# Kernel optimization log

Hardware: AMD Instinct MI355X
Metric: run time of the kernel (lower is better)

The kernel has to match this reference:

```python
import jax, jax.numpy as jnp
import numpy as np

L, D, H, F, V, B, S = 4, 256, 8, 2048, 1024, 4, 1024
HD = D // H
EPS = 1e-5
PARAM_NAMES = ['enc_qkv_w','enc_qkv_b','enc_out_w','enc_out_b','enc_ff1_w','enc_ff1_b','enc_ff2_w','enc_ff2_b','enc_ln1_g','enc_ln1_b','enc_ln2_g','enc_ln2_b','dec_sa_qkv_w','dec_sa_qkv_b','dec_sa_out_w','dec_sa_out_b','dec_ca_qkv_w','dec_ca_qkv_b','dec_ca_out_w','dec_ca_out_b','dec_ff1_w','dec_ff1_b','dec_ff2_w','dec_ff2_b','dec_ln1_g','dec_ln1_b','dec_ln2_g','dec_ln2_b','dec_ln3_g','dec_ln3_b']

def _ln(x, g, b):
    m = jnp.mean(x, -1, keepdims=True)
    v = jnp.mean((x - m) ** 2, -1, keepdims=True)
    return (x - m) * jax.lax.rsqrt(v + EPS) * g + b

def _mha(q_in, kv_in, qkv_w, qkv_b, out_w, out_b, key_mask=None):
    wq, wk, wv = jnp.split(qkv_w, 3, axis=0)
    bq, bk, bv = jnp.split(qkv_b, 3, axis=0)
    q = (q_in @ wq.T + bq).reshape(q_in.shape[0], -1, H, HD)
    k = (kv_in @ wk.T + bk).reshape(kv_in.shape[0], -1, H, HD)
    v = (kv_in @ wv.T + bv).reshape(kv_in.shape[0], -1, H, HD)
    scores = jnp.einsum('bqhd,bkhd->bhqk', q, k) / np.float32(np.sqrt(HD))
    if key_mask is not None:
        scores = jnp.where(key_mask[:, None, None, :], jnp.float32(-1e9), scores)
    attn = jax.nn.softmax(scores, axis=-1)
    o = jnp.einsum('bhqk,bkhd->bqhd', attn, v).reshape(q_in.shape[0], -1, D)
    return o @ out_w.T + out_b

def _forward(x, mask, codebook, pos, p):
    h = codebook[x] + pos[:, :x.shape[1], :]  # [B,S,D]
    # --- bidirectional encoder (post-LN, ReLU FFN, torch defaults) ---
    ctx = h
    for l in range(L):
        sa = _mha(ctx, ctx, p['enc_qkv_w'][l], p['enc_qkv_b'][l], p['enc_out_w'][l], p['enc_out_b'][l], mask)
        ctx = _ln(ctx + sa, p['enc_ln1_g'][l], p['enc_ln1_b'][l])
        ff = jax.nn.relu(ctx @ p['enc_ff1_w'][l].T + p['enc_ff1_b'][l]) @ p['enc_ff2_w'][l].T + p['enc_ff2_b'][l]
        ctx = _ln(ctx + ff, p['enc_ln2_g'][l], p['enc_ln2_b'][l])
    # --- depth decoder: original loops per position with tgt len 1.
    # Self-attn over a single token == out_proj(v_proj(x)); cross-attn over the
    # shared context is independent per position, so all S positions batch exactly. ---
    d = h
    for l in range(L):
        wv = p['dec_sa_qkv_w'][l][2 * D:]
        bv = p['dec_sa_qkv_b'][l][2 * D:]
        sa = (d @ wv.T + bv) @ p['dec_sa_out_w'][l].T + p['dec_sa_out_b'][l]
        d = _ln(d + sa, p['dec_ln1_g'][l], p['dec_ln1_b'][l])
        ca = _mha(d, ctx, p['dec_ca_qkv_w'][l], p['dec_ca_qkv_b'][l], p['dec_ca_out_w'][l], p['dec_ca_out_b'][l])
        d = _ln(d + ca, p['dec_ln2_g'][l], p['dec_ln2_b'][l])
        ff = jax.nn.relu(d @ p['dec_ff1_w'][l].T + p['dec_ff1_b'][l]) @ p['dec_ff2_w'][l].T + p['dec_ff2_b'][l]
        d = _ln(d + ff, p['dec_ln3_g'][l], p['dec_ln3_b'][l])
    return d

def setup_inputs() -> dict:
    key = jax.random.key(0)
    ctr = [0]
    def nk():
        k = jax.random.fold_in(key, ctr[0]); ctr[0] += 1; return k
    def prm(shape):
        return jax.random.normal(nk(), shape, jnp.float32) * 0.02
    inp = {
        'x': jax.random.randint(nk(), (B, S), 0, V),
        'mask': jnp.zeros((B, S), bool),
        'codebook': prm((V, D)),
        'pos': prm((1, V, D)),
        'enc_qkv_w': prm((L, 3 * D, D)), 'enc_qkv_b': jnp.zeros((L, 3 * D)),
        'enc_out_w': prm((L, D, D)), 'enc_out_b': jnp.zeros((L, D)),
        'enc_ff1_w': prm((L, F, D)), 'enc_ff1_b': jnp.zeros((L, F)),
        'enc_ff2_w': prm((L, D, F)), 'enc_ff2_b': jnp.zeros((L, D)),
        'enc_ln1_g': jnp.ones((L, D)), 'enc_ln1_b': jnp.zeros((L, D)),
        'enc_ln2_g': jnp.ones((L, D)), 'enc_ln2_b': jnp.zeros((L, D)),
        'dec_sa_qkv_w': prm((L, 3 * D, D)), 'dec_sa_qkv_b': jnp.zeros((L, 3 * D)),
        'dec_sa_out_w': prm((L, D, D)), 'dec_sa_out_b': jnp.zeros((L, D)),
        'dec_ca_qkv_w': prm((L, 3 * D, D)), 'dec_ca_qkv_b': jnp.zeros((L, 3 * D)),
        'dec_ca_out_w': prm((L, D, D)), 'dec_ca_out_b': jnp.zeros((L, D)),
        'dec_ff1_w': prm((L, F, D)), 'dec_ff1_b': jnp.zeros((L, F)),
        'dec_ff2_w': prm((L, D, F)), 'dec_ff2_b': jnp.zeros((L, D)),
        'dec_ln1_g': jnp.ones((L, D)), 'dec_ln1_b': jnp.zeros((L, D)),
        'dec_ln2_g': jnp.ones((L, D)), 'dec_ln2_b': jnp.zeros((L, D)),
        'dec_ln3_g': jnp.ones((L, D)), 'dec_ln3_b': jnp.zeros((L, D)),
    }
    return inp

def reference(x, mask, codebook, pos, enc_qkv_w, enc_qkv_b, enc_out_w, enc_out_b, enc_ff1_w, enc_ff1_b, enc_ff2_w, enc_ff2_b, enc_ln1_g, enc_ln1_b, enc_ln2_g, enc_ln2_b, dec_sa_qkv_w, dec_sa_qkv_b, dec_sa_out_w, dec_sa_out_b, dec_ca_qkv_w, dec_ca_qkv_b, dec_ca_out_w, dec_ca_out_b, dec_ff1_w, dec_ff1_b, dec_ff2_w, dec_ff2_b, dec_ln1_g, dec_ln1_b, dec_ln2_g, dec_ln2_b, dec_ln3_g, dec_ln3_b):
    vals = (enc_qkv_w, enc_qkv_b, enc_out_w, enc_out_b, enc_ff1_w, enc_ff1_b, enc_ff2_w, enc_ff2_b, enc_ln1_g, enc_ln1_b, enc_ln2_g, enc_ln2_b, dec_sa_qkv_w, dec_sa_qkv_b, dec_sa_out_w, dec_sa_out_b, dec_ca_qkv_w, dec_ca_qkv_b, dec_ca_out_w, dec_ca_out_b, dec_ff1_w, dec_ff1_b, dec_ff2_w, dec_ff2_b, dec_ln1_g, dec_ln1_b, dec_ln2_g, dec_ln2_b, dec_ln3_g, dec_ln3_b)
    p = dict(zip(PARAM_NAMES, vals))
    return _forward(x, mask, codebook, pos, p)
```

## Files before the change

### kernel.cpp

```cpp
#include <hip/hip_runtime.h>

typedef unsigned short u16;
typedef unsigned int   u32;
typedef short short8 __attribute__((ext_vector_type(8)));
typedef float f32x4  __attribute__((ext_vector_type(4)));

#define DEV static __device__ __forceinline__

static constexpr int S_ = 1024;
static constexpr int D_ = 256;
static constexpr int NR = 4096;

DEV u16 f2bf(float x) {
    u32 u = __float_as_uint(x);
    return (u16)((u + 0x7FFFu + ((u >> 16) & 1u)) >> 16);
}
DEV float bf2f(u16 s) { return __uint_as_float(((u32)s) << 16); }


__global__ __launch_bounds__(256) void k_fillf(float* __restrict__ o, int n, float v) {
    int i = blockIdx.x * 256 + threadIdx.x;
    if (i < n) o[i] = v;
}

__global__ __launch_bounds__(256) void k_conv_all(
        const float* __restrict__ s0, const float* __restrict__ s1, const float* __restrict__ s2,
        const float* __restrict__ s3, const float* __restrict__ s4, const float* __restrict__ s5,
        const float* __restrict__ s6, const float* __restrict__ s7, const float* __restrict__ s8,
        const float* __restrict__ s9, u16* __restrict__ dst) {
    constexpr int c0 = 786432/4,            c1 = c0 + 262144/4,  c2 = c1 + 2097152/4,
                  c3 = c2 + 2097152/4,      c4 = c3 + 786432/4,  c5 = c4 + 262144/4,
                  c6 = c5 + 786432/4,       c7 = c6 + 262144/4,  c8 = c7 + 2097152/4,
                  c9 = c8 + 2097152/4;
    for (int i = blockIdx.x * 256 + threadIdx.x; i < c9; i += gridDim.x * 256) {
        const float* src; int base;
        if      (i < c0) { src = s0; base = 0;  }
        else if (i < c1) { src = s1; base = c0; }
        else if (i < c2) { src = s2; base = c1; }
        else if (i < c3) { src = s3; base = c2; }
        else if (i < c4) { src = s4; base = c3; }
        else if (i < c5) { src = s5; base = c4; }
        else if (i < c6) { src = s6; base = c5; }
        else if (i < c7) { src = s7; base = c6; }
        else if (i < c8) { src = s8; base = c7; }
        else             { src = s9; base = c8; }
        float4 v = ((const float4*)src)[i - base];
        ushort4 o; o.x = f2bf(v.x); o.y = f2bf(v.y); o.z = f2bf(v.z); o.w = f2bf(v.w);
        ((ushort4*)dst)[i] = o;
    }
}

__global__ __launch_bounds__(256) void k_wsa(const float* __restrict__ qkvw, const float* __restrict__ qkvb,
                                             const float* __restrict__ outw, const float* __restrict__ outb,
                                             u16* __restrict__ wsa, float* __restrict__ bsa) {
    int l = blockIdx.x >> 8, n = blockIdx.x & 255, t = threadIdx.x;
    const float* wv = qkvw + (size_t)l * 196608 + 131072;
    const float* bv = qkvb + l * 768 + 512;
    const float* wo = outw + (size_t)l * 65536 + n * 256;
    float acc = 0.0f, pb = 0.0f;
    for (int j = 0; j < 256; j++) {
        float woj = wo[j];
        acc = fmaf(woj, wv[j * 256 + t], acc);
        pb  = fmaf(woj, bv[j], pb);
    }
    wsa[(size_t)l * 65536 + n * 256 + t] = f2bf(acc);
    if (t == 0) bsa[l * 256 + n] = pb + outb[l * 256 + n];
}

__global__ __launch_bounds__(256) void k_embed(const int* __restrict__ xx,
                                               const float* __restrict__ cb,
                                               const float* __restrict__ pos,
                                               const unsigned char* __restrict__ mask,
                                               float* __restrict__ hf, u16* __restrict__ hb,
                                               float* __restrict__ av, float* __restrict__ avz) {
    int wid = threadIdx.x >> 6, lane = threadIdx.x & 63;
    int row = blockIdx.x * 4 + wid;
    int sp = row & (S_ - 1);
    int tok = xx[row];
    float4 c = ((const float4*)(cb + (size_t)tok * D_))[lane];
    float4 p = ((const float4*)(pos + (size_t)sp * D_))[lane];
    float4 s; s.x = c.x + p.x; s.y = c.y + p.y; s.z = c.z + p.z; s.w = c.w + p.w;
    ((float4*)(hf + (size_t)row * D_))[lane] = s;
    ushort4 o; o.x = f2bf(s.x); o.y = f2bf(s.y); o.z = f2bf(s.z); o.w = f2bf(s.w);
    ((ushort4*)(hb + (size_t)row * D_))[lane] = o;
    if (lane == 0) { av[row] = mask[row] ? -2.0e9f : 0.0f; avz[row] = 0.0f; }
}

__global__ __launch_bounds__(256) void k_ln4(const float* __restrict__ x, const u16* __restrict__ yp,
                                             const float* __restrict__ gg, const float* __restrict__ bb,
                                             float* __restrict__ of, u16* __restrict__ ob) {
    int wid = threadIdx.x >> 6, lane = threadIdx.x & 63;
    int row = blockIdx.x * 4 + wid;
    float4 xv = ((const float4*)(x + (size_t)row * D_))[lane];
    float4 s = xv;
    #pragma unroll
    for (int kz = 0; kz < 4; kz++) {
        ushort4 yv = ((const ushort4*)(yp + (size_t)kz * NR * D_ + (size_t)row * D_))[lane];
        s.x += bf2f(yv.x); s.y += bf2f(yv.y); s.z += bf2f(yv.z); s.w += bf2f(yv.w);
    }
    float sum = s.x + s.y + s.z + s.w;
    float sq  = s.x * s.x + s.y * s.y + s.z * s.z + s.w * s.w;
    #pragma unroll
    for (int m = 1; m < 64; m <<= 1) { sum += __shfl_xor(sum, m, 64); sq += __shfl_xor(sq, m, 64); }
    float mean = sum * (1.0f / 256.0f);
    float var  = sq * (1.0f / 256.0f) - mean * mean;
    float rs = rsqrtf(var + 1e-5f);
    float4 gv = ((const float4*)gg)[lane];
    float4 bv = ((const float4*)bb)[lane];
    float4 o;
    o.x = (s.x - mean) * rs * gv.x + bv.x;
    o.y = (s.y - mean) * rs * gv.y + bv.y;
    o.z = (s.z - mean) * rs * gv.z + bv.z;
    o.w = (s.w - mean) * rs * gv.w + bv.w;
    ((float4*)(of + (size_t)row * D_))[lane] = o;
    ushort4 ub; ub.x = f2bf(o.x); ub.y = f2bf(o.y); ub.z = f2bf(o.z); ub.w = f2bf(o.w);
    ((ushort4*)(ob + (size_t)row * D_))[lane] = ub;
}


template <int BM, int BN, bool RELU, bool OBF16>
__global__ __launch_bounds__(256) void k_gemm(const u16* __restrict__ A, const u16* __restrict__ Bw,
                                              const float* __restrict__ bias,
                                              float* __restrict__ Cf, u16* __restrict__ Cb,
                                              int Nn, int Kk) {
    constexpr int FM = BM / 32, FN = BN / 32;
    constexpr int LDA = 72;
    __shared__ __align__(16) u16 As[BM * LDA];
    __shared__ __align__(16) u16 Bs[BN * LDA];
    int tid = threadIdx.x, w = tid >> 6, lane = tid & 63;
    int lr = lane & 15, g = lane >> 4;
    int wm = w >> 1, wn = w & 1;
    int nbn = Nn / BN;
    int bid = blockIdx.x, nwg = gridDim.x;
    if ((nwg & 7) == 0) bid = (bid & 7) * (nwg >> 3) + (bid >> 3);
    int m0 = (bid / nbn) * BM, n0 = (bid % nbn) * BN;
    int trow = tid >> 3, tcol = (tid & 7) << 3;

    f32x4 acc[FM][FN] = {};

    for (int kb = 0; kb < Kk; kb += 64) {
        if (kb) __syncthreads();
        #pragma unroll
        for (int r = 0; r < BM / 32; r++) {
            int row = r * 32 + trow;
            uint4 v = *(const uint4*)(A + (size_t)(m0 + row) * Kk + kb + tcol);
            *(uint4*)(As + row * LDA + tcol) = v;
        }
        #pragma unroll
        for (int r = 0; r < BN / 32; r++) {
            int row = r * 32 + trow;
            uint4 v = *(const uint4*)(Bw + (size_t)(n0 + row) * Kk + kb + tcol);
            *(uint4*)(Bs + row * LDA + tcol) = v;
        }
        __syncthreads();
        #pragma unroll
        for (int kk = 0; kk < 2; kk++) {
            short8 af[FM], bfr[FN];
            #pragma unroll
            for (int mi = 0; mi < FM; mi++)
                af[mi] = *(const short8*)(As + (wm * (BM / 2) + mi * 16 + lr) * LDA + kk * 32 + g * 8);
            #pragma unroll
            for (int ni = 0; ni < FN; ni++)
                bfr[ni] = *(const short8*)(Bs + (wn * (BN / 2) + ni * 16 + lr) * LDA + kk * 32 + g * 8);
            #pragma unroll
            for (int mi = 0; mi < FM; mi++)
                #pragma unroll
                for (int ni = 0; ni < FN; ni++)
                    acc[mi][ni] = __builtin_amdgcn_mfma_f32_16x16x32_bf16(af[mi], bfr[ni], acc[mi][ni], 0, 0, 0);
        }
    }

    #pragma unroll
    for (int ni = 0; ni < FN; ni++) {
        int col = n0 + wn * (BN / 2) + ni * 16 + lr;
        float bi = bias[col];
        #pragma unroll
        for (int mi = 0; mi < FM; mi++) {
            #pragma unroll
            for (int jj = 0; jj < 4; jj++) {
                int row = m0 + wm * (BM / 2) + mi * 16 + g * 4 + jj;
                float v = acc[mi][ni][jj] + bi;
                if (RELU) v = fmaxf(v, 0.0f);
                if (OBF16) Cb[(size_t)row * Nn + col] = f2bf(v);
                else       Cf[(size_t)row * Nn + col] = v;
            }
        }
    }
}

__global__ __launch_bounds__(256) void k_gemm_ln(const u16* __restrict__ A, const u16* __restrict__ Bw,
                                                 const float* __restrict__ bias,
                                                 const float* __restrict__ resid,
                                                 const float* __restrict__ gg, const float* __restrict__ bb,
                                                 float* __restrict__ of, u16* __restrict__ ob) {
    constexpr int LDA = 72, Kk = 256;
    __shared__ __align__(16) u16 As[16 * LDA];
    __shared__ __align__(16) u16 Bs[256 * LDA];
    int tid = threadIdx.x, w = tid >> 6, lane = tid & 63;
    int lr = lane & 15, g = lane >> 4;
    int bid = blockIdx.x;
    bid = (bid & 7) * 32 + (bid >> 3);
    int m0 = bid * 16;
    int trow = tid >> 3, tcol = (tid & 7) << 3;

    f32x4 acc[4] = {};

    for (int kb = 0; kb < Kk; kb += 64) {
        if (kb) __syncthreads();
        if (tid < 128) {
            int row = tid >> 3;
            uint4 v = *(const uint4*)(A + (size_t)(m0 + row) * Kk + kb + tcol);
            *(uint4*)(As + row * LDA + tcol) = v;
        }
        #pragma unroll
        for (int r = 0; r < 8; r++) {
            int row = r * 32 + trow;
            uint4 v = *(const uint4*)(Bw + (size_t)row * Kk + kb + tcol);
            *(uint4*)(Bs + row * LDA + tcol) = v;
        }
        __syncthreads();
        #pragma unroll
        for (int kk = 0; kk < 2; kk++) {
            short8 af = *(const short8*)(As + lr * LDA + kk * 32 + g * 8);
            #pragma unroll
            for (int ni = 0; ni < 4; ni++) {
                short8 bfr = *(const short8*)(Bs + (w * 64 + ni * 16 + lr) * LDA + kk * 32 + g * 8);
                acc[ni] = __builtin_amdgcn_mfma_f32_16x16x32_bf16(af, bfr, acc[ni], 0, 0, 0);
            }
        }
    }

    __syncthreads();
    float* Cs = (float*)Bs;
    #pragma unroll
    for (int ni = 0; ni < 4; ni++) {
        int col = w * 64 + ni * 16 + lr;
        float bi = bias[col];
        #pragma unroll
        for (int jj = 0; jj < 4; jj++)
            Cs[(g * 4 + jj) * 260 + col] = acc[ni][jj] + bi;
    }
    __syncthreads();

    int row = tid >> 4, c0 = (tid & 15) * 16;
    float v[16];
    float sum = 0.0f, sq = 0.0f;
    #pragma unroll
    for (int i = 0; i < 4; i++) {
        float4 cv = *(float4*)(Cs + row * 260 + c0 + i * 4);
        float4 rv = *(const float4*)(resid + (size_t)(m0 + row) * D_ + c0 + i * 4);
        v[4*i]   = cv.x + rv.x; v[4*i+1] = cv.y + rv.y;
        v[4*i+2] = cv.z + rv.z; v[4*i+3] = cv.w + rv.w;
    }
    #pragma unroll
    for (int i = 0; i < 16; i++) { sum += v[i]; sq += v[i] * v[i]; }
    #pragma unroll
    for (int m = 1; m < 16; m <<= 1) { sum += __shfl_xor(sum, m, 64); sq += __shfl_xor(sq, m, 64); }
    float mean = sum * (1.0f / 256.0f);
    float var  = sq * (1.0f / 256.0f) - mean * mean;
    float rs = rsqrtf(var + 1e-5f);
    float* op = of + (size_t)(m0 + row) * D_ + c0;
    u16*   bp = ob + (size_t)(m0 + row) * D_ + c0;
    #pragma unroll
    for (int i = 0; i < 4; i++) {
        float4 gv = *(const float4*)(gg + c0 + i * 4);
        float4 bv = *(const float4*)(bb + c0 + i * 4);
        float4 o;
        o.x = (v[4*i]   - mean) * rs * gv.x + bv.x;
        o.y = (v[4*i+1] - mean) * rs * gv.y + bv.y;
        o.z = (v[4*i+2] - mean) * rs * gv.z + bv.z;
        o.w = (v[4*i+3] - mean) * rs * gv.w + bv.w;
        *(float4*)(op + i * 4) = o;
        ushort4 ub; ub.x = f2bf(o.x); ub.y = f2bf(o.y); ub.z = f2bf(o.z); ub.w = f2bf(o.w);
        *(ushort4*)(bp + i * 4) = ub;
    }
}

__global__ __launch_bounds__(256) void k_gemm2(const u16* __restrict__ A0, const u16* __restrict__ W0,
                                               const float* __restrict__ b0, u16* __restrict__ C0,
                                               const u16* __restrict__ A1, const u16* __restrict__ W1,
                                               const float* __restrict__ b1, u16* __restrict__ C1) {
    constexpr int LDA = 72, Kk = 256;
    __shared__ __align__(16) u16 As[64 * LDA];
    __shared__ __align__(16) u16 Bs[64 * LDA];
    int tid = threadIdx.x, w = tid >> 6, lane = tid & 63;
    int lr = lane & 15, g = lane >> 4;
    int wm = w >> 1, wn = w & 1;
    int bid = blockIdx.x;
    bid = (bid & 7) * 96 + (bid >> 3);
    const u16 *A, *Bw; const float* bias; u16* Cb; int Nn, nbn, seg;
    if (bid < 256) { A = A0; Bw = W0; bias = b0; Cb = C0; Nn = 256; nbn = 4; seg = bid; }
    else           { A = A1; Bw = W1; bias = b1; Cb = C1; Nn = 512; nbn = 8; seg = bid - 256; }
    int m0 = (seg / nbn) * 64, n0 = (seg % nbn) * 64;
    int trow = tid >> 3, tcol = (tid & 7) << 3;

    f32x4 acc[2][2] = {};

    for (int kb = 0; kb < Kk; kb += 64) {
        if (kb) __syncthreads();
        #pragma unroll
        for (int r = 0; r < 2; r++) {
            int row = r * 32 + trow;
            uint4 va = *(const uint4*)(A + (size_t)(m0 + row) * Kk + kb + tcol);
            *(uint4*)(As + row * LDA + tcol) = va;
            uint4 vb = *(const uint4*)(Bw + (size_t)(n0 + row) * Kk + kb + tcol);
            *(uint4*)(Bs + row * LDA + tcol) = vb;
        }
        __syncthreads();
        #pragma unroll
        for (int kk = 0; kk < 2; kk++) {
            short8 af[2], bfr[2];
            #pragma unroll
            for (int mi = 0; mi < 2; mi++)
                af[mi] = *(const short8*)(As + (wm * 32 + mi * 16 + lr) * LDA + kk * 32 + g * 8);
            #pragma unroll
            for (int ni = 0; ni < 2; ni++)
                bfr[ni] = *(const short8*)(Bs + (wn * 32 + ni * 16 + lr) * LDA + kk * 32 + g * 8);
            #pragma unroll
            for (int mi = 0; mi < 2; mi++)
                #pragma unroll
                for (int ni = 0; ni < 2; ni++)
                    acc[mi][ni] = __builtin_amdgcn_mfma_f32_16x16x32_bf16(af[mi], bfr[ni], acc[mi][ni], 0, 0, 0);
        }
    }

    #pragma unroll
    for (int ni = 0; ni < 2; ni++) {
        int col = n0 + wn * 32 + ni * 16 + lr;
        float bi = bias[col];
        #pragma unroll
        for (int mi = 0; mi < 2; mi++)
            #pragma unroll
            for (int jj = 0; jj < 4; jj++) {
                int row = m0 + wm * 32 + mi * 16 + g * 4 + jj;
                Cb[(size_t)row * Nn + col] = f2bf(acc[mi][ni][jj] + bi);
            }
    }
}

__global__ __launch_bounds__(256) void k_gemm_sk4(const u16* __restrict__ A, const u16* __restrict__ Bw,
                                                  const float* __restrict__ bias, u16* __restrict__ Cp) {
    constexpr int LDA = 72, Nn = 256, Kk = 2048;
    __shared__ __align__(16) u16 As[64 * LDA];
    __shared__ __align__(16) u16 Bs[64 * LDA];
    int tid = threadIdx.x, w = tid >> 6, lane = tid & 63;
    int lr = lane & 15, g = lane >> 4;
    int wm = w >> 1, wn = w & 1;
    int kz = blockIdx.x >> 8;
    int mn = blockIdx.x & 255;
    mn = (mn & 7) * 32 + (mn >> 3);
    int m0 = (mn >> 2) * 64, n0 = (mn & 3) * 64;
    int kbeg = kz * 512;
    int trow = tid >> 3, tcol = (tid & 7) << 3;

    f32x4 acc[2][2] = {};

    for (int kb = kbeg; kb < kbeg + 512; kb += 64) {
        if (kb != kbeg) __syncthreads();
        #pragma unroll
        for (int r = 0; r < 2; r++) {
            int row = r * 32 + trow;
            uint4 va = *(const uint4*)(A + (size_t)(m0 + row) * Kk + kb + tcol);
            *(uint4*)(As + row * LDA + tcol) = va;
            uint4 vb = *(const uint4*)(Bw + (size_t)(n0 + row) * Kk + kb + tcol);
            *(uint4*)(Bs + row * LDA + tcol) = vb;
        }
        __syncthreads();
        #pragma unroll
        for (int kk = 0; kk < 2; kk++) {
            short8 af[2], bfr[2];
            #pragma unroll
            for (int mi = 0; mi < 2; mi++)
                af[mi] = *(const short8*)(As + (wm * 32 + mi * 16 + lr) * LDA + kk * 32 + g * 8);
            #pragma unroll
            for (int ni = 0; ni < 2; ni++)
                bfr[ni] = *(const short8*)(Bs + (wn * 32 + ni * 16 + lr) * LDA + kk * 32 + g * 8);
            #pragma unroll
            for (int mi = 0; mi < 2; mi++)
                #pragma unroll
                for (int ni = 0; ni < 2; ni++)
                    acc[mi][ni] = __builtin_amdgcn_mfma_f32_16x16x32_bf16(af[mi], bfr[ni], acc[mi][ni], 0, 0, 0);
        }
    }

    u16* Cz = Cp + (size_t)kz * NR * Nn;
    #pragma unroll
    for (int ni = 0; ni < 2; ni++) {
        int col = n0 + wn * 32 + ni * 16 + lr;
        float bi = (kz == 0) ? bias[col] : 0.0f;
        #pragma unroll
        for (int mi = 0; mi < 2; mi++)
            #pragma unroll
            for (int jj = 0; jj < 4; jj++) {
                int row = m0 + wm * 32 + mi * 16 + g * 4 + jj;
                Cz[(size_t)row * Nn + col] = f2bf(acc[mi][ni][jj] + bi);
            }
    }
}


__global__ __launch_bounds__(256) void k_attn(const u16* __restrict__ qp, int qs,
                                              const u16* __restrict__ kvp, int ks, int koff, int voff,
                                              const float* __restrict__ addv, u16* __restrict__ out) {
    __shared__ __align__(16) u16 Kl[2][128 * 32];
    __shared__ __align__(16) u16 VTl[2][32 * 136];
    __shared__ __align__(16) u16 Pl[4 * 16 * 136];
    __shared__ float Al[2][128];

    int tid = threadIdx.x, w = tid >> 6, lane = tid & 63;
    int lr = lane & 15, g = lane >> 4;
    int blk = blockIdx.x;
    blk = (blk & 7) * 64 + (blk >> 3);
    int qb = blk & 15, h = (blk >> 4) & 7, b = blk >> 7;
    int q0 = qb * 64 + w * 16;
    const float QS2 = 0.17677669529663687f * 1.4426950408889634f;

    short8 qf = *(const short8*)(qp + (size_t)(b * S_ + q0 + lr) * qs + h * 32 + g * 8);

    f32x4 o0 = {0.f, 0.f, 0.f, 0.f}, o1 = {0.f, 0.f, 0.f, 0.f};
    float m_run = -3.0e38f, l_run = 0.0f;
    float sreg[8][4];
    u16* Pw = Pl + w * 16 * 136;

    int key_t = tid >> 1, dh = (tid & 1) * 16;
    const u16* kbase = kvp + (size_t)(b * S_) * ks;

    uint4 ka0, ka1;
    union { uint4 v[2]; u16 s[16]; } vu;
    float alv = 0.0f;
    auto ldregs = [&](int kb) {
        const u16* srck = kbase + (size_t)(kb * 128 + key_t) * ks + koff + h * 32 + dh;
        ka0 = *(const uint4*)srck;
        ka1 = *(const uint4*)(srck + 8);
        const u16* srcv = kbase + (size_t)(kb * 128 + key_t) * ks + voff + h * 32 + dh;
        vu.v[0] = *(const uint4*)srcv;
        vu.v[1] = *(const uint4*)(srcv + 8);
        if (tid < 128) alv = addv[b * S_ + kb * 128 + tid];
    };
    auto stbuf = [&](int buf) {
        *(uint4*)(&Kl[buf][key_t * 32 + dh])     = ka0;
        *(uint4*)(&Kl[buf][key_t * 32 + dh + 8]) = ka1;
        #pragma unroll
        for (int i = 0; i < 16; i++) VTl[buf][(dh + i) * 136 + key_t] = vu.s[i];
        if (tid < 128) Al[buf][tid] = alv;
    };

    ldregs(0); stbuf(0);
    int cur = 0;
    for (int kb = 0; kb < 8; kb++) {
        __syncthreads();

        #pragma unroll
        for (int t = 0; t < 8; t++) {
            short8 kf = *(const short8*)(&Kl[cur][(t * 16 + lr) * 32 + g * 8]);
            f32x4 z = {0.f, 0.f, 0.f, 0.f};
            f32x4 st = __builtin_amdgcn_mfma_f32_16x16x32_bf16(kf, qf, z, 0, 0, 0);
            #pragma unroll
            for (int jj = 0; jj < 4; jj++) sreg[t][jj] = st[jj] * QS2 + Al[cur][t * 16 + g * 4 + jj];
        }

        if (kb < 7) ldregs(kb + 1);

        float mb = -3.0e38f;
        #pragma unroll
        for (int t = 0; t < 8; t++)
            #pragma unroll
            for (int jj = 0; jj < 4; jj++) mb = fmaxf(mb, sreg[t][jj]);
        mb = fmaxf(mb, __shfl_xor(mb, 16, 64));
        mb = fmaxf(mb, __shfl_xor(mb, 32, 64));
        float mnew = fmaxf(m_run, mb);
        float sc = __builtin_amdgcn_exp2f(m_run - mnew);
        float ls = 0.f;
        #pragma unroll
        for (int t = 0; t < 8; t++)
            #pragma unroll
            for (int jj = 0; jj < 4; jj++) {
                float p = __builtin_amdgcn_exp2f(sreg[t][jj] - mnew);
                sreg[t][jj] = p; ls += p;
            }
        ls += __shfl_xor(ls, 16, 64); ls += __shfl_xor(ls, 32, 64);
        l_run = l_run * sc + ls; m_run = mnew;
        #pragma unroll
        for (int jj = 0; jj < 4; jj++) {
            float scj = __shfl(sc, 20 * g + jj, 64);
            o0[jj] *= scj; o1[jj] *= scj;
        }

        #pragma unroll
        for (int t = 0; t < 8; t++) {
            u32 u0 = (u32)f2bf(sreg[t][0]) | ((u32)f2bf(sreg[t][1]) << 16);
            u32 u1 = (u32)f2bf(sreg[t][2]) | ((u32)f2bf(sreg[t][3]) << 16);
            *(uint2*)(Pw + lr * 136 + t * 16 + g * 4) = make_uint2(u0, u1);
        }

        #pragma unroll
        for (int c = 0; c < 4; c++) {
            short8 pa = *(const short8*)(Pw + lr * 136 + c * 32 + g * 8);
            short8 v0 = *(const short8*)(&VTl[cur][lr * 136 + c * 32 + g * 8]);
            short8 v1 = *(const short8*)(&VTl[cur][(16 + lr) * 136 + c * 32 + g * 8]);
            o0 = __builtin_amdgcn_mfma_f32_16x16x32_bf16(pa, v0, o0, 0, 0, 0);
            o1 = __builtin_amdgcn_mfma_f32_16x16x32_bf16(pa, v1, o1, 0, 0, 0);
        }

        __syncthreads();
        if (kb < 7) stbuf(cur ^ 1);
        cur ^= 1;
    }

    float li = 1.0f / l_run;
    #pragma unroll
    for (int jj = 0; jj < 4; jj++) {
        float lij = __shfl(li, 20 * g + jj, 64);
        int r = q0 + g * 4 + jj;
        u16* op = out + (size_t)(b * S_ + r) * 256 + h * 32;
        op[lr]      = f2bf(o0[jj] * lij);
        op[16 + lr] = f2bf(o1[jj] * lij);
    }
}


extern "C" void kernel_launch(void* const* d_in, const int* in_sizes, int n_in,
                              void* d_out, int out_size, void* d_ws, size_t ws_size,
                              hipStream_t stream) {
    const int* x                = (const int*)d_in[0];
    const unsigned char* mask   = (const unsigned char*)d_in[1];
    const float* codebook       = (const float*)d_in[2];
    const float* pos            = (const float*)d_in[3];
    const float* enc_qkv_w = (const float*)d_in[4];  const float* enc_qkv_b = (const float*)d_in[5];
    const float* enc_out_w = (const float*)d_in[6];  const float* enc_out_b = (const float*)d_in[7];
    const float* enc_ff1_w = (const float*)d_in[8];  const float* enc_ff1_b = (const float*)d_in[9];
    const float* enc_ff2_w = (const float*)d_in[10]; const float* enc_ff2_b = (const float*)d_in[11];
    const float* enc_ln1_g = (const float*)d_in[12]; const float* enc_ln1_b = (const float*)d_in[13];
    const float* enc_ln2_g = (const float*)d_in[14]; const float* enc_ln2_b = (const float*)d_in[15];
    const float* dec_sa_qkv_w = (const float*)d_in[16]; const float* dec_sa_qkv_b = (const float*)d_in[17];
    const float* dec_sa_out_w = (const float*)d_in[18]; const float* dec_sa_out_b = (const float*)d_in[19];
    const float* dec_ca_qkv_w = (const float*)d_in[20]; const float* dec_ca_qkv_b = (const float*)d_in[21];
    const float* dec_ca_out_w = (const float*)d_in[22]; const float* dec_ca_out_b = (const float*)d_in[23];
    const float* dec_ff1_w = (const float*)d_in[24]; const float* dec_ff1_b = (const float*)d_in[25];
    const float* dec_ff2_w = (const float*)d_in[26]; const float* dec_ff2_b = (const float*)d_in[27];
    const float* dec_ln1_g = (const float*)d_in[28]; const float* dec_ln1_b = (const float*)d_in[29];
    const float* dec_ln2_g = (const float*)d_in[30]; const float* dec_ln2_b = (const float*)d_in[31];
    const float* dec_ln3_g = (const float*)d_in[32]; const float* dec_ln3_b = (const float*)d_in[33];

    char* ws = (char*)d_ws; size_t off = 0;
    auto alloc = [&](size_t b) { char* p = ws + off; off += (b + 255) & ~(size_t)255; return p; };

    u16* w_eqkv  = (u16*)alloc((size_t)786432 * 2);
    u16* w_eout  = (u16*)alloc((size_t)262144 * 2);
    u16* w_eff1  = (u16*)alloc((size_t)2097152 * 2);
    u16* w_eff2  = (u16*)alloc((size_t)2097152 * 2);
    u16* w_dsaq  = (u16*)alloc((size_t)786432 * 2);
    u16* w_dsao  = (u16*)alloc((size_t)262144 * 2);
    u16* w_dcaq  = (u16*)alloc((size_t)786432 * 2);
    u16* w_dcao  = (u16*)alloc((size_t)262144 * 2);
    u16* w_dff1  = (u16*)alloc((size_t)2097152 * 2);
    u16* w_dff2  = (u16*)alloc((size_t)2097152 * 2);
    u16*   wsa   = (u16*)  alloc((size_t)4 * 65536 * 2);
    float* bsa   = (float*)alloc((size_t)4 * 256 * 4);
    float* h_f   = (float*)alloc((size_t)NR * D_ * 4);
    u16*   h_b   = (u16*)  alloc((size_t)NR * D_ * 2);
    float* ctx_f = (float*)alloc((size_t)NR * D_ * 4);
    u16*   ctx_b = (u16*)  alloc((size_t)NR * D_ * 2);
    float* dd_f  = (float*)alloc((size_t)NR * D_ * 4);
    u16*   dd_b  = (u16*)  alloc((size_t)NR * D_ * 2);
    u16*   gem_p = (u16*)  alloc((size_t)4 * NR * 256 * 2);
    u16*   attno = (u16*)  alloc((size_t)NR * 256 * 2);
    float* addv  = (float*)alloc((size_t)NR * 4);
    float* addvz = (float*)alloc((size_t)NR * 4);
    u16* scr = (u16*)alloc((size_t)NR * 2048 * 2);
    u16* qkv_b = scr;
    u16* ffh_b = scr;
    u16* qca_b = scr;
    u16* kvca_b = scr + (size_t)NR * 256;
    (void)in_sizes; (void)n_in;

    if (off > ws_size) {
        k_fillf<<<(out_size + 255) / 256, 256, 0, stream>>>((float*)d_out, out_size, 1000.0f);
        return;
    }

    k_conv_all<<<2048, 256, 0, stream>>>(enc_qkv_w, enc_out_w, enc_ff1_w, enc_ff2_w,
                                         dec_sa_qkv_w, dec_sa_out_w, dec_ca_qkv_w, dec_ca_out_w,
                                         dec_ff1_w, dec_ff2_w, w_eqkv);
    k_wsa<<<1024, 256, 0, stream>>>(dec_sa_qkv_w, dec_sa_qkv_b, dec_sa_out_w, dec_sa_out_b, wsa, bsa);
    k_embed<<<1024, 256, 0, stream>>>(x, codebook, pos, mask, h_f, h_b, addv, addvz);

    for (int l = 0; l < 4; l++) {
        const u16* inb = l ? ctx_b : h_b;
        const float* inf = l ? ctx_f : h_f;
        k_gemm<64,64,false,true><<<768, 256, 0, stream>>>(inb, w_eqkv + (size_t)l*196608,
            enc_qkv_b + l*768, nullptr, qkv_b, 768, 256);
        k_attn<<<512, 256, 0, stream>>>(qkv_b, 768, qkv_b, 768, 256, 512, addv, attno);
        k_gemm_ln<<<256, 256, 0, stream>>>(attno, w_eout + (size_t)l*65536, enc_out_b + l*256,
            inf, enc_ln1_g + l*256, enc_ln1_b + l*256, ctx_f, ctx_b);
        k_gemm<128,128,true,true><<<512, 256, 0, stream>>>(ctx_b, w_eff1 + (size_t)l*524288,
            enc_ff1_b + l*2048, nullptr, ffh_b, 2048, 256);
        k_gemm_sk4<<<1024, 256, 0, stream>>>(ffh_b, w_eff2 + (size_t)l*524288,
            enc_ff2_b + l*256, gem_p);
        k_ln4<<<1024, 256, 0, stream>>>(ctx_f, gem_p, enc_ln2_g + l*256, enc_ln2_b + l*256, ctx_f, ctx_b);
    }

    for (int l = 0; l < 4; l++) {
        const u16* inb = l ? dd_b : h_b;
        const float* inf = l ? dd_f : h_f;
        k_gemm_ln<<<256, 256, 0, stream>>>(inb, wsa + (size_t)l*65536, bsa + l*256,
            inf, dec_ln1_g + l*256, dec_ln1_b + l*256, dd_f, dd_b);
        k_gemm2<<<768, 256, 0, stream>>>(dd_b, w_dcaq + (size_t)l*196608, dec_ca_qkv_b + l*768, qca_b,
                                         ctx_b, w_dcaq + (size_t)l*196608 + 65536,
                                         dec_ca_qkv_b + l*768 + 256, kvca_b);
        k_attn<<<512, 256, 0, stream>>>(qca_b, 256, kvca_b, 512, 0, 256, addvz, attno);
        k_gemm_ln<<<256, 256, 0, stream>>>(attno, w_dcao + (size_t)l*65536, dec_ca_out_b + l*256,
            dd_f, dec_ln2_g + l*256, dec_ln2_b + l*256, dd_f, dd_b);
        k_gemm<128,128,true,true><<<512, 256, 0, stream>>>(dd_b, w_dff1 + (size_t)l*524288,
            dec_ff1_b + l*2048, nullptr, ffh_b, 2048, 256);
        k_gemm_sk4<<<1024, 256, 0, stream>>>(ffh_b, w_dff2 + (size_t)l*524288,
            dec_ff2_b + l*256, gem_p);
        k_ln4<<<1024, 256, 0, stream>>>(dd_f, gem_p, dec_ln3_g + l*256, dec_ln3_b + l*256,
                                        (l == 3) ? (float*)d_out : dd_f, dd_b);
    }
}
```

Baseline: 579.6 us.

## Fuse prep kernels into one launch and drop attention loop barrier

Merges the weight-conversion, fused self-attention weight precompute and embedding kernels into a single launch, with the block index choosing which job a block does. This saves two kernel launches and lets the three independent jobs run side by side. In the attention kernel the next K/V tile is now staged before the P·V MFMAs, and the __syncthreads at the end of each iteration is removed. With only two buffers and no barrier, a fast wave may overwrite a buffer that other waves are still reading, which risks a race and wrong results.

```diff
diff --git a/kernel.cpp b/kernel.cpp
--- a/kernel.cpp
+++ b/kernel.cpp
@@ -23,67 +23,66 @@
     if (i < n) o[i] = v;
 }
 
-__global__ __launch_bounds__(256) void k_conv_all(
+__global__ __launch_bounds__(256) void k_prep(
         const float* __restrict__ s0, const float* __restrict__ s1, const float* __restrict__ s2,
         const float* __restrict__ s3, const float* __restrict__ s4, const float* __restrict__ s5,
         const float* __restrict__ s6, const float* __restrict__ s7, const float* __restrict__ s8,
-        const float* __restrict__ s9, u16* __restrict__ dst) {
-    constexpr int c0 = 786432/4,            c1 = c0 + 262144/4,  c2 = c1 + 2097152/4,
-                  c3 = c2 + 2097152/4,      c4 = c3 + 786432/4,  c5 = c4 + 262144/4,
-                  c6 = c5 + 786432/4,       c7 = c6 + 262144/4,  c8 = c7 + 2097152/4,
-                  c9 = c8 + 2097152/4;
-    for (int i = blockIdx.x * 256 + threadIdx.x; i < c9; i += gridDim.x * 256) {
-        const float* src; int base;
-        if      (i < c0) { src = s0; base = 0;  }
-        else if (i < c1) { src = s1; base = c0; }
-        else if (i < c2) { src = s2; base = c1; }
-        else if (i < c3) { src = s3; base = c2; }
-        else if (i < c4) { src = s4; base = c3; }
-        else if (i < c5) { src = s5; base = c4; }
-        else if (i < c6) { src = s6; base = c5; }
-        else if (i < c7) { src = s7; base = c6; }
-        else if (i < c8) { src = s8; base = c7; }
-        else             { src = s9; base = c8; }
-        float4 v = ((const float4*)src)[i - base];
-        ushort4 o; o.x = f2bf(v.x); o.y = f2bf(v.y); o.z = f2bf(v.z); o.w = f2bf(v.w);
-        ((ushort4*)dst)[i] = o;
-    }
-}
-
-__global__ __launch_bounds__(256) void k_wsa(const float* __restrict__ qkvw, const float* __restrict__ qkvb,
-                                             const float* __restrict__ outw, const float* __restrict__ outb,
-                                             u16* __restrict__ wsa, float* __restrict__ bsa) {
-    int l = blockIdx.x >> 8, n = blockIdx.x & 255, t = threadIdx.x;
-    const float* wv = qkvw + (size_t)l * 196608 + 131072;
-    const float* bv = qkvb + l * 768 + 512;
-    const float* wo = outw + (size_t)l * 65536 + n * 256;
-    float acc = 0.0f, pb = 0.0f;
-    for (int j = 0; j < 256; j++) {
-        float woj = wo[j];
-        acc = fmaf(woj, wv[j * 256 + t], acc);
-        pb  = fmaf(woj, bv[j], pb);
-    }
-    wsa[(size_t)l * 65536 + n * 256 + t] = f2bf(acc);
-    if (t == 0) bsa[l * 256 + n] = pb + outb[l * 256 + n];
-}
-
-__global__ __launch_bounds__(256) void k_embed(const int* __restrict__ xx,
-                                               const float* __restrict__ cb,
-                                               const float* __restrict__ pos,
-                                               const unsigned char* __restrict__ mask,
-                                               float* __restrict__ hf, u16* __restrict__ hb,
-                                               float* __restrict__ av, float* __restrict__ avz) {
-    int wid = threadIdx.x >> 6, lane = threadIdx.x & 63;
-    int row = blockIdx.x * 4 + wid;
-    int sp = row & (S_ - 1);
-    int tok = xx[row];
-    float4 c = ((const float4*)(cb + (size_t)tok * D_))[lane];
-    float4 p = ((const float4*)(pos + (size_t)sp * D_))[lane];
-    float4 s; s.x = c.x + p.x; s.y = c.y + p.y; s.z = c.z + p.z; s.w = c.w + p.w;
-    ((float4*)(hf + (size_t)row * D_))[lane] = s;
-    ushort4 o; o.x = f2bf(s.x); o.y = f2bf(s.y); o.z = f2bf(s.z); o.w = f2bf(s.w);
-    ((ushort4*)(hb + (size_t)row * D_))[lane] = o;
-    if (lane == 0) { av[row] = mask[row] ? -2.0e9f : 0.0f; avz[row] = 0.0f; }
+        const float* __restrict__ s9, u16* __restrict__ dst,
+        const float* __restrict__ saqw, const float* __restrict__ saqb,
+        const float* __restrict__ saow, const float* __restrict__ saob,
+        u16* __restrict__ wsa, float* __restrict__ bsa,
+        const int* __restrict__ xx, const float* __restrict__ cb, const float* __restrict__ pos,
+        const unsigned char* __restrict__ mask,
+        float* __restrict__ hf, u16* __restrict__ hb,
+        float* __restrict__ av, float* __restrict__ avz) {
+    int bid = blockIdx.x, t = threadIdx.x;
+    if (bid < 2048) {
+        constexpr int c0 = 786432/4,            c1 = c0 + 262144/4,  c2 = c1 + 2097152/4,
+                      c3 = c2 + 2097152/4,      c4 = c3 + 786432/4,  c5 = c4 + 262144/4,
+                      c6 = c5 + 786432/4,       c7 = c6 + 262144/4,  c8 = c7 + 2097152/4,
+                      c9 = c8 + 2097152/4;
+        for (int i = bid * 256 + t; i < c9; i += 2048 * 256) {
+            const float* src; int base;
+            if      (i < c0) { src = s0; base = 0;  }
+            else if (i < c1) { src = s1; base = c0; }
+            else if (i < c2) { src = s2; base = c1; }
+            else if (i < c3) { src = s3; base = c2; }
+            else if (i < c4) { src = s4; base = c3; }
+            else if (i < c5) { src = s5; base = c4; }
+            else if (i < c6) { src = s6; base = c5; }
+            else if (i < c7) { src = s7; base = c6; }
+            else if (i < c8) { src = s8; base = c7; }
+            else             { src = s9; base = c8; }
+            float4 v = ((const float4*)src)[i - base];
+            ushort4 o; o.x = f2bf(v.x); o.y = f2bf(v.y); o.z = f2bf(v.z); o.w = f2bf(v.w);
+            ((ushort4*)dst)[i] = o;
+        }
+    } else if (bid < 3072) {
+        int l = (bid - 2048) >> 8, n = (bid - 2048) & 255;
+        const float* wv = saqw + (size_t)l * 196608 + 131072;
+        const float* bv = saqb + l * 768 + 512;
+        const float* wo = saow + (size_t)l * 65536 + n * 256;
+        float acc = 0.0f, pb = 0.0f;
+        for (int j = 0; j < 256; j++) {
+            float woj = wo[j];
+            acc = fmaf(woj, wv[j * 256 + t], acc);
+            pb  = fmaf(woj, bv[j], pb);
+        }
+        wsa[(size_t)l * 65536 + n * 256 + t] = f2bf(acc);
+        if (t == 0) bsa[l * 256 + n] = pb + saob[l * 256 + n];
+    } else {
+        int wid = t >> 6, lane = t & 63;
+        int row = (bid - 3072) * 4 + wid;
+        int sp = row & (S_ - 1);
+        int tok = xx[row];
+        float4 c = ((const float4*)(cb + (size_t)tok * D_))[lane];
+        float4 p = ((const float4*)(pos + (size_t)sp * D_))[lane];
+        float4 s; s.x = c.x + p.x; s.y = c.y + p.y; s.z = c.z + p.z; s.w = c.w + p.w;
+        ((float4*)(hf + (size_t)row * D_))[lane] = s;
+        ushort4 o; o.x = f2bf(s.x); o.y = f2bf(s.y); o.z = f2bf(s.z); o.w = f2bf(s.w);
+        ((ushort4*)(hb + (size_t)row * D_))[lane] = o;
+        if (lane == 0) { av[row] = mask[row] ? -2.0e9f : 0.0f; avz[row] = 0.0f; }
+    }
 }
 
 __global__ __launch_bounds__(256) void k_ln4(const float* __restrict__ x, const u16* __restrict__ yp,
@@ -493,6 +492,8 @@
             *(uint2*)(Pw + lr * 136 + t * 16 + g * 4) = make_uint2(u0, u1);
         }
 
+        if (kb < 7) stbuf(cur ^ 1);
+
         #pragma unroll
         for (int c = 0; c < 4; c++) {
             short8 pa = *(const short8*)(Pw + lr * 136 + c * 32 + g * 8);
@@ -502,8 +503,6 @@
             o1 = __builtin_amdgcn_mfma_f32_16x16x32_bf16(pa, v1, o1, 0, 0, 0);
         }
 
-        __syncthreads();
-        if (kb < 7) stbuf(cur ^ 1);
         cur ^= 1;
     }
 
@@ -579,11 +578,11 @@
         return;
     }
 
-    k_conv_all<<<2048, 256, 0, stream>>>(enc_qkv_w, enc_out_w, enc_ff1_w, enc_ff2_w,
-                                         dec_sa_qkv_w, dec_sa_out_w, dec_ca_qkv_w, dec_ca_out_w,
-                                         dec_ff1_w, dec_ff2_w, w_eqkv);
-    k_wsa<<<1024, 256, 0, stream>>>(dec_sa_qkv_w, dec_sa_qkv_b, dec_sa_out_w, dec_sa_out_b, wsa, bsa);
-    k_embed<<<1024, 256, 0, stream>>>(x, codebook, pos, mask, h_f, h_b, addv, addvz);
+    k_prep<<<4096, 256, 0, stream>>>(enc_qkv_w, enc_out_w, enc_ff1_w, enc_ff2_w,
+                                     dec_sa_qkv_w, dec_sa_out_w, dec_ca_qkv_w, dec_ca_out_w,
+                                     dec_ff1_w, dec_ff2_w, w_eqkv,
+                                     dec_sa_qkv_w, dec_sa_qkv_b, dec_sa_out_w, dec_sa_out_b, wsa, bsa,
+                                     x, codebook, pos, mask, h_f, h_b, addv, addvz);
 
     for (int l = 0; l < 4; l++) {
         const u16* inb = l ? ctx_b : h_b;
```

Result: no change. 575.8 us (-0.7%).
